# Kernel tuning notes

Hardware: AMD Instinct MI355X
Metric: run time of the kernel (lower is better)

The kernel has to match this reference:

```python
import jax, jax.numpy as jnp
import numpy as np

N = 50000   # nodes
E = 500000  # edges
H = 128     # hidden_dim


def setup_inputs() -> dict:
    key = jax.random.key(0)
    ks = jax.random.split(key, 8)
    w = lambda k, shp: jax.random.normal(k, shp, jnp.float32) * 0.02
    return {
        "edge_idx": jax.random.randint(ks[0], (E, 2), 0, N, dtype=jnp.int32),
        "node_feats": jax.random.normal(ks[1], (N, H), jnp.float32),
        "edge_feats": jax.random.normal(ks[2], (E, H), jnp.float32),
        # edge MLP params: Linear(3H,H) -> ReLU -> Linear(H,H) -> LayerNorm(H)
        "We1": w(ks[3], (3 * H, H)), "be1": jnp.zeros((H,), jnp.float32),
        "We2": w(ks[4], (H, H)),     "be2": jnp.zeros((H,), jnp.float32),
        "ge": jnp.ones((H,), jnp.float32), "bge": jnp.zeros((H,), jnp.float32),
        # node MLP params: Linear(2H,H) -> ReLU -> Linear(H,H) -> LayerNorm(H)
        "Wn1": w(ks[5], (2 * H, H)), "bn1": jnp.zeros((H,), jnp.float32),
        "Wn2": w(ks[6], (H, H)),     "bn2": jnp.zeros((H,), jnp.float32),
        "gn": jnp.ones((H,), jnp.float32), "bgn": jnp.zeros((H,), jnp.float32),
    }


def layer_norm(x, g, b, eps=1e-5):
    m = jnp.mean(x, axis=-1, keepdims=True)
    v = jnp.var(x, axis=-1, keepdims=True)
    return (x - m) * jax.lax.rsqrt(v + eps) * g + b


def reference(edge_idx, node_feats, edge_feats,
              We1, be1, We2, be2, ge, bge,
              Wn1, bn1, Wn2, bn2, gn, bgn):
    senders = edge_idx[:, 0]
    receivers = edge_idx[:, 1]
    # edge update: gather endpoints, concat with edge feats, MLP + LN
    e_in = jnp.concatenate([node_feats[senders], node_feats[receivers], edge_feats], axis=-1)  # [E, 3H]
    edge_update = layer_norm(jax.nn.relu(e_in @ We1 + be1) @ We2 + be2, ge, bge)               # [E, H]
    # faithful to source: scatter-add of edge_feats (NOT edge_update) into receivers
    acc = jax.ops.segment_sum(edge_feats, receivers, num_segments=node_feats.shape[0])          # [N, H]
    n_in = jnp.concatenate([node_feats, acc], axis=-1)                                          # [N, 2H]
    node_update = layer_norm(jax.nn.relu(n_in @ Wn1 + bn1) @ Wn2 + bn2, gn, bgn)                # [N, H]
    return node_feats + node_update, edge_feats + edge_update
```

## Files before the change

### kernel.cpp

```cpp
#include <hip/hip_runtime.h>
#include <hip/hip_bf16.h>

#define DI __device__ __forceinline__

typedef __attribute__((ext_vector_type(8))) short short8;
typedef __attribute__((ext_vector_type(4))) short short4v;
typedef __attribute__((ext_vector_type(4))) float floatx4;

constexpr int NN = 50000;
constexpr int NE = 500000;
constexpr int H  = 128;
constexpr int NB1 = (NN + 255) / 256;

constexpr size_t OFF_BF   = 229376;
constexpr size_t OFF_PS   = 294912;
constexpr size_t OFF_PR   = 13094912;
constexpr size_t OFF_CNT  = 25894912;
constexpr size_t OFF_TMP  = 26094912;
constexpr size_t OFF_RS   = 26294912;
constexpr size_t OFF_CUR  = 26494912;
constexpr size_t OFF_BSUM = 26694912;
constexpr size_t OFF_CSR  = 26695936;

constexpr int WF_TOTAL = 114688;
constexpr int BIASF_FLOATS = 8*2048;

DI short f2bf(float f){ __bf16 b = (__bf16)f; return __builtin_bit_cast(short, b); }
DI float bf2f(short s){ return __builtin_bit_cast(float, ((unsigned)(unsigned short)s) << 16); }

__global__ __launch_bounds__(256) void zero_cnt_kernel(int* __restrict__ cnt){
  int i = blockIdx.x*256 + threadIdx.x;
  if (i < NN) cnt[i] = 0;
}

__global__ __launch_bounds__(256) void prep_kernel(
    const float* __restrict__ We1, const float* __restrict__ We2,
    const float* __restrict__ Wn1, const float* __restrict__ Wn2,
    const float* __restrict__ be1, const float* __restrict__ be2,
    const float* __restrict__ ge,  const float* __restrict__ bge,
    const float* __restrict__ bn1, const float* __restrict__ bn2,
    const float* __restrict__ gn,  const float* __restrict__ bgn,
    short* __restrict__ wf, float* __restrict__ bf)
{
  int t = blockIdx.x*256 + threadIdx.x;
  if (t < WF_TOTAL) {
    int blk = t >> 14, u = t & 16383;
    int j = u & 7, l = (u>>3)&63, nt = (u>>9)&7, ks = u>>12;
    const float* src; int roff;
    switch (blk) {
      case 0: src = We1; roff = 0;   break;
      case 1: src = We1; roff = 128; break;
      case 2: src = We1; roff = 256; break;
      case 3: src = We2; roff = 0;   break;
      case 4: src = Wn1; roff = 0;   break;
      case 5: src = Wn1; roff = 128; break;
      default: src = Wn2; roff = 0;  break;
    }
    int row = roff + 32*ks + 8*(l>>4) + j;
    int col = 16*nt + (l&15);
    wf[t] = f2bf(src[row*H + col]);
  } else if (t < WF_TOTAL + BIASF_FLOATS) {
    int tb = t - WF_TOTAL;
    int arr = tb >> 11, u = tb & 2047;
    int r = u&3, l = (u>>2)&63, mt = u>>8;
    int feat = 16*mt + 4*(l>>4) + r;
    const float* s;
    switch (arr) {
      case 0: s = be1; break; case 1: s = be2; break;
      case 2: s = ge;  break; case 3: s = bge; break;
      case 4: s = bn1; break; case 5: s = bn2; break;
      case 6: s = gn;  break; default: s = bgn; break;
    }
    bf[tb] = s[feat];
  }
}

__global__ __launch_bounds__(256) void hist_kernel(const int* __restrict__ ei, int* __restrict__ cnt){
  int e = blockIdx.x*256 + threadIdx.x;
  if (e < NE) atomicAdd(&cnt[ei[2*e+1]], 1);
}

__global__ __launch_bounds__(256) void scan1_kernel(const int* __restrict__ cnt,
                                                    int* __restrict__ tmp, int* __restrict__ blocksum){
  __shared__ int s[256];
  int t = threadIdx.x, i = blockIdx.x*256 + t;
  int v = (i < NN) ? cnt[i] : 0;
  s[t] = v; __syncthreads();
#pragma unroll
  for (int o=1; o<256; o<<=1){
    int u = (t >= o) ? s[t-o] : 0;
    __syncthreads();
    s[t] += u;
    __syncthreads();
  }
  if (i < NN) tmp[i] = s[t];
  if (t == 255) blocksum[blockIdx.x] = s[255];
}

__global__ __launch_bounds__(256) void scan2_kernel(int* __restrict__ blocksum){
  __shared__ int s[256];
  int t = threadIdx.x;
  int v = (t < NB1) ? blocksum[t] : 0;
  s[t] = v; __syncthreads();
#pragma unroll
  for (int o=1; o<256; o<<=1){
    int u = (t >= o) ? s[t-o] : 0;
    __syncthreads();
    s[t] += u;
    __syncthreads();
  }
  if (t < NB1) blocksum[t] = s[t] - v;
}

__global__ __launch_bounds__(256) void scan3_kernel(const int* __restrict__ cnt, const int* __restrict__ tmp,
                                                    const int* __restrict__ blocksum,
                                                    int* __restrict__ rowstart, int* __restrict__ cursor){
  int i = blockIdx.x*256 + threadIdx.x;
  if (i < NN){
    int rs = tmp[i] - cnt[i] + blocksum[blockIdx.x];
    rowstart[i] = rs; cursor[i] = rs;
  }
}

__global__ __launch_bounds__(256) void scatter_kernel(const int* __restrict__ ei,
                                                      int* __restrict__ cursor, int* __restrict__ csr){
  int e = blockIdx.x*256 + threadIdx.x;
  if (e < NE){
    int r = ei[2*e+1];
    int p = atomicAdd(&cursor[r], 1);
    csr[p] = e;
  }
}

__global__ __launch_bounds__(256) void segsum_kernel(const int* __restrict__ csr,
                                                     const int* __restrict__ rowstart,
                                                     const int* __restrict__ cnt,
                                                     const float* __restrict__ edge_feats,
                                                     float* __restrict__ acc){
  int tid = threadIdx.x;
  int w = tid>>6, l = tid&63;
  int hh = l>>5, q = l&31;
  int n = blockIdx.x*8 + w*2 + hh;
  if (n >= NN) return;
  int start = rowstart[n], deg = cnt[n];
  floatx4 s = floatx4{0.f,0.f,0.f,0.f};
  int k = 0;
  for (; k+4 <= deg; k += 4){
    int e0 = csr[start+k],   e1 = csr[start+k+1];
    int e2 = csr[start+k+2], e3 = csr[start+k+3];
    floatx4 v0 = *(const floatx4*)(edge_feats + (size_t)e0*H + 4*q);
    floatx4 v1 = *(const floatx4*)(edge_feats + (size_t)e1*H + 4*q);
    floatx4 v2 = *(const floatx4*)(edge_feats + (size_t)e2*H + 4*q);
    floatx4 v3 = *(const floatx4*)(edge_feats + (size_t)e3*H + 4*q);
    s += v0; s += v1; s += v2; s += v3;
  }
  for (; k < deg; ++k){
    int e = csr[start+k];
    s += *(const floatx4*)(edge_feats + (size_t)e*H + 4*q);
  }
  *(floatx4*)(acc + (size_t)n*H + 4*q) = s;
}

__global__ __launch_bounds__(256) void pproj_kernel(
    const float* __restrict__ node_feats,
    const short* __restrict__ wsf, const short* __restrict__ wrf,
    const float* __restrict__ b1f,
    short* __restrict__ Ps, short* __restrict__ Pr)
{
  const int tid = threadIdx.x;
  const int w = tid>>6, l = tid&63, g = l>>4, lo = l&15;
  int row = blockIdx.x*64 + w*16 + lo;
  bool valid = row < NN;
  int rowc = valid ? row : (NN-1);
  const float* sp = node_feats + (size_t)rowc*H;

  short8 ein[4];
#pragma unroll
  for (int ks=0; ks<4; ++ks){
    const int koff = ks*32 + g*8;
    floatx4 f0 = *(const floatx4*)(sp + koff);
    floatx4 f1 = *(const floatx4*)(sp + koff + 4);
    ein[ks][0]=f2bf(f0[0]); ein[ks][1]=f2bf(f0[1]); ein[ks][2]=f2bf(f0[2]); ein[ks][3]=f2bf(f0[3]);
    ein[ks][4]=f2bf(f1[0]); ein[ks][5]=f2bf(f1[1]); ein[ks][6]=f2bf(f1[2]); ein[ks][7]=f2bf(f1[3]);
  }

  floatx4 as[8], ar[8];
#pragma unroll
  for (int mt=0; mt<8; ++mt){ as[mt] = floatx4{0,0,0,0}; ar[mt] = floatx4{0,0,0,0}; }
#pragma unroll
  for (int ks=0; ks<4; ++ks){
#pragma unroll
    for (int mt=0; mt<8; ++mt){
      short8 wv = *(const short8*)(wsf + ((ks*8+mt)*64 + l)*8);
      as[mt] = __builtin_amdgcn_mfma_f32_16x16x32_bf16(wv, ein[ks], as[mt], 0,0,0);
      short8 wv2 = *(const short8*)(wrf + ((ks*8+mt)*64 + l)*8);
      ar[mt] = __builtin_amdgcn_mfma_f32_16x16x32_bf16(wv2, ein[ks], ar[mt], 0,0,0);
    }
  }

  if (valid){
    short* ps = Ps + (size_t)rowc*H + g*32;
    short* pr = Pr + (size_t)rowc*H + g*32;
#pragma unroll
    for (int mt=0; mt<8; ++mt){
      floatx4 bv = *(const floatx4*)(b1f + (mt*64+l)*4);
      short4v vs, vr;
#pragma unroll
      for (int r=0; r<4; ++r){ vs[r] = f2bf(as[mt][r] + bv[r]); vr[r] = f2bf(ar[mt][r]); }
      *(short4v*)(ps + mt*4) = vs;
      *(short4v*)(pr + mt*4) = vr;
    }
  }
}

template<int R>
__global__ __launch_bounds__(256, 4) void edge_kernel(
    const int* __restrict__ edge_idx,
    const float* __restrict__ edge_feats,
    const short* __restrict__ Ps, const short* __restrict__ Pr,
    const short* __restrict__ wef, const short* __restrict__ w2f,
    const float* __restrict__ b2f,
    const float* __restrict__ gf,  const float* __restrict__ bgf,
    float* __restrict__ out_edge)
{
  __shared__ short lds_h[4*R*2048];
  const int tid = threadIdx.x;
  const int w = tid>>6, l = tid&63, g = l>>4, lo = l&15;

  int rowc[R]; bool valid[R]; int2 se[R];
#pragma unroll
  for (int b=0; b<R; ++b){
    int row = blockIdx.x*(64*R) + w*(16*R) + b*16 + lo;
    valid[b] = row < NE;
    rowc[b]  = valid[b] ? row : (NE-1);
    se[b] = *(const int2*)(edge_idx + 2*rowc[b]);
  }

  short8 vs[4], vr[4];
  {
    const short* ps = Ps + (size_t)se[0].x*H + g*32;
    const short* pr = Pr + (size_t)se[0].y*H + g*32;
#pragma unroll
    for (int m2=0; m2<4; ++m2){
      vs[m2] = *(const short8*)(ps + m2*8);
      vr[m2] = *(const short8*)(pr + m2*8);
    }
  }

#pragma unroll
  for (int b=0; b<R; ++b){
    floatx4 acc1[8];
#pragma unroll
    for (int mt=0; mt<8; ++mt) acc1[mt] = floatx4{0.f,0.f,0.f,0.f};

    const float* sp = edge_feats + (size_t)rowc[b]*H;
#pragma unroll
    for (int ks=0; ks<4; ++ks){
      const int koff = ks*32 + g*8;
      floatx4 f0 = *(const floatx4*)(sp + koff);
      floatx4 f1 = *(const floatx4*)(sp + koff + 4);
      short8 ein;
      ein[0]=f2bf(f0[0]); ein[1]=f2bf(f0[1]); ein[2]=f2bf(f0[2]); ein[3]=f2bf(f0[3]);
      ein[4]=f2bf(f1[0]); ein[5]=f2bf(f1[1]); ein[6]=f2bf(f1[2]); ein[7]=f2bf(f1[3]);
#pragma unroll
      for (int mt=0; mt<8; ++mt){
        short8 wv = *(const short8*)(wef + ((ks*8+mt)*64 + l)*8);
        acc1[mt] = __builtin_amdgcn_mfma_f32_16x16x32_bf16(wv, ein, acc1[mt], 0,0,0);
      }
    }

#pragma unroll
    for (int m2=0; m2<4; ++m2)
#pragma unroll
      for (int r=0; r<4; ++r){
        acc1[2*m2][r]   += bf2f(vs[m2][r])   + bf2f(vr[m2][r]);
        acc1[2*m2+1][r] += bf2f(vs[m2][4+r]) + bf2f(vr[m2][4+r]);
      }

    if (b+1 < R){
      const short* ps = Ps + (size_t)se[b+1].x*H + g*32;
      const short* pr = Pr + (size_t)se[b+1].y*H + g*32;
#pragma unroll
      for (int m2=0; m2<4; ++m2){
        vs[m2] = *(const short8*)(ps + m2*8);
        vr[m2] = *(const short8*)(pr + m2*8);
      }
    }

    short* ldsw = lds_h + (w*R + b)*2048;
#pragma unroll
    for (int mt=0; mt<8; ++mt){
      short4v hv;
#pragma unroll
      for (int r=0; r<4; ++r){
        float v = acc1[mt][r];
        hv[r] = f2bf(v > 0.f ? v : 0.f);
      }
      int off = (lo*256 + mt*32 + g*8) ^ ((lo&7)<<4);
      *(short4v*)((char*)ldsw + off) = hv;
    }
  }

  floatx4 acc2[R][8];
#pragma unroll
  for (int mt=0; mt<8; ++mt){
    floatx4 bv = *(const floatx4*)(b2f + (mt*64+l)*4);
#pragma unroll
    for (int b=0; b<R; ++b) acc2[b][mt] = bv;
  }

#pragma unroll
  for (int s=0; s<4; ++s){
    short8 hb[R];
#pragma unroll
    for (int b=0; b<R; ++b){
      short* ldsw = lds_h + (w*R + b)*2048;
      int roff = (lo*256 + s*64 + g*16) ^ ((lo&7)<<4);
      hb[b] = *(const short8*)((char*)ldsw + roff);
    }
#pragma unroll
    for (int mt=0; mt<8; ++mt){
      short8 wv = *(const short8*)(w2f + ((s*8+mt)*64 + l)*8);
#pragma unroll
      for (int b=0; b<R; ++b)
        acc2[b][mt] = __builtin_amdgcn_mfma_f32_16x16x32_bf16(wv, hb[b], acc2[b][mt], 0,0,0);
    }
  }

  float meanv[R], rsv[R];
#pragma unroll
  for (int b=0; b<R; ++b){
    float sum = 0.f, ssq = 0.f;
#pragma unroll
    for (int mt=0; mt<8; ++mt)
#pragma unroll
      for (int r=0; r<4; ++r){ float v = acc2[b][mt][r]; sum += v; ssq += v*v; }
    sum += __shfl_xor(sum, 16); ssq += __shfl_xor(ssq, 16);
    sum += __shfl_xor(sum, 32); ssq += __shfl_xor(ssq, 32);
    meanv[b] = sum * (1.f/H);
    float var = ssq * (1.f/H) - meanv[b]*meanv[b];
    rsv[b] = rsqrtf(var + 1e-5f);
  }

#pragma unroll
  for (int mt=0; mt<8; ++mt){
    floatx4 gv  = *(const floatx4*)(gf  + (mt*64+l)*4);
    floatx4 bgv = *(const floatx4*)(bgf + (mt*64+l)*4);
#pragma unroll
    for (int b=0; b<R; ++b){
      const float* resid = edge_feats + (size_t)rowc[b]*H;
      floatx4 ef = *(const floatx4*)(resid + mt*16 + g*4);
      floatx4 o;
#pragma unroll
      for (int r=0; r<4; ++r) o[r] = ef[r] + (acc2[b][mt][r]-meanv[b])*rsv[b]*gv[r] + bgv[r];
      if (valid[b]) *(floatx4*)(out_edge + (size_t)rowc[b]*H + mt*16 + g*4) = o;
    }
  }
}

__global__ __launch_bounds__(256) void node_kernel(
    const float* __restrict__ node_feats,
    const short* __restrict__ w1f, const short* __restrict__ w2f,
    const float* __restrict__ b1f, const float* __restrict__ b2f,
    const float* __restrict__ gf,  const float* __restrict__ bgf,
    float* __restrict__ out_node)
{
  __shared__ short lds_h[4*2048];
  const int tid = threadIdx.x;
  const int w = tid>>6, l = tid&63, g = l>>4, lo = l&15;
  short* ldsw = lds_h + w*2048;

  int row = blockIdx.x*64 + w*16 + lo;
  bool valid = row < NN;
  int rowc = valid ? row : (NN-1);
  const float* sp0 = node_feats + (size_t)rowc*H;
  const float* sp1 = out_node   + (size_t)rowc*H;

  floatx4 acc1[8];
#pragma unroll
  for (int mt=0; mt<8; ++mt) acc1[mt] = *(const floatx4*)(b1f + (mt*64+l)*4);

#pragma unroll
  for (int ks=0; ks<8; ++ks){
    const float* sp = (ks<4) ? sp0 : sp1;
    const int koff = (ks&3)*32 + g*8;
    floatx4 f0 = *(const floatx4*)(sp + koff);
    floatx4 f1 = *(const floatx4*)(sp + koff + 4);
    short8 ein;
    ein[0]=f2bf(f0[0]); ein[1]=f2bf(f0[1]); ein[2]=f2bf(f0[2]); ein[3]=f2bf(f0[3]);
    ein[4]=f2bf(f1[0]); ein[5]=f2bf(f1[1]); ein[6]=f2bf(f1[2]); ein[7]=f2bf(f1[3]);
#pragma unroll
    for (int mt=0; mt<8; ++mt){
      short8 wv = *(const short8*)(w1f + ((ks*8+mt)*64 + l)*8);
      acc1[mt] = __builtin_amdgcn_mfma_f32_16x16x32_bf16(wv, ein, acc1[mt], 0,0,0);
    }
  }

#pragma unroll
  for (int mt=0; mt<8; ++mt){
    short4v hv;
#pragma unroll
    for (int r=0; r<4; ++r){
      float v = acc1[mt][r];
      hv[r] = f2bf(v > 0.f ? v : 0.f);
    }
    int off = (lo*256 + mt*32 + g*8) ^ ((lo&7)<<4);
    *(short4v*)((char*)ldsw + off) = hv;
  }

  floatx4 acc2[8];
#pragma unroll
  for (int mt=0; mt<8; ++mt) acc2[mt] = *(const floatx4*)(b2f + (mt*64+l)*4);

#pragma unroll
  for (int s=0; s<4; ++s){
    int roff = (lo*256 + s*64 + g*16) ^ ((lo&7)<<4);
    short8 hb = *(const short8*)((char*)ldsw + roff);
#pragma unroll
    for (int mt=0; mt<8; ++mt){
      short8 wv = *(const short8*)(w2f + ((s*8+mt)*64 + l)*8);
      acc2[mt] = __builtin_amdgcn_mfma_f32_16x16x32_bf16(wv, hb, acc2[mt], 0,0,0);
    }
  }

  float sum = 0.f, ssq = 0.f;
#pragma unroll
  for (int mt=0; mt<8; ++mt)
#pragma unroll
    for (int r=0; r<4; ++r){ float v = acc2[mt][r]; sum += v; ssq += v*v; }
  sum += __shfl_xor(sum, 16); ssq += __shfl_xor(ssq, 16);
  sum += __shfl_xor(sum, 32); ssq += __shfl_xor(ssq, 32);
  const float mean = sum * (1.f/H);
  const float var  = ssq * (1.f/H) - mean*mean;
  const float rs   = rsqrtf(var + 1e-5f);

#pragma unroll
  for (int mt=0; mt<8; ++mt){
    floatx4 gv  = *(const floatx4*)(gf  + (mt*64+l)*4);
    floatx4 bgv = *(const floatx4*)(bgf + (mt*64+l)*4);
    floatx4 nf  = *(const floatx4*)(node_feats + (size_t)rowc*H + mt*16 + g*4);
    floatx4 o;
#pragma unroll
    for (int r=0; r<4; ++r) o[r] = nf[r] + (acc2[mt][r]-mean)*rs*gv[r] + bgv[r];
    if (valid) *(floatx4*)(out_node + (size_t)rowc*H + mt*16 + g*4) = o;
  }
}

extern "C" void kernel_launch(void* const* d_in, const int* in_sizes, int n_in,
                              void* d_out, int out_size, void* d_ws, size_t ws_size,
                              hipStream_t stream)
{
  const int*   edge_idx   = (const int*)  d_in[0];
  const float* node_feats = (const float*)d_in[1];
  const float* edge_feats = (const float*)d_in[2];
  const float* We1=(const float*)d_in[3];  const float* be1=(const float*)d_in[4];
  const float* We2=(const float*)d_in[5];  const float* be2=(const float*)d_in[6];
  const float* ge =(const float*)d_in[7];  const float* bge=(const float*)d_in[8];
  const float* Wn1=(const float*)d_in[9];  const float* bn1=(const float*)d_in[10];
  const float* Wn2=(const float*)d_in[11]; const float* bn2=(const float*)d_in[12];
  const float* gn =(const float*)d_in[13]; const float* bgn=(const float*)d_in[14];

  float* out_node = (float*)d_out;
  float* out_edge = out_node + (size_t)NN*H;

  char* ws = (char*)d_ws;
  short* wf      = (short*)ws;
  float* bf      = (float*)(ws + OFF_BF);
  short* Ps      = (short*)(ws + OFF_PS);
  short* Pr      = (short*)(ws + OFF_PR);
  int* cnt       = (int*)(ws + OFF_CNT);
  int* tmp       = (int*)(ws + OFF_TMP);
  int* rowstart  = (int*)(ws + OFF_RS);
  int* cursor    = (int*)(ws + OFF_CUR);
  int* blocksum  = (int*)(ws + OFF_BSUM);
  int* csr       = (int*)(ws + OFF_CSR);

  short* wsf  = wf;
  short* wrf  = wf + 16384;
  short* wef  = wf + 32768;
  short* w2f  = wf + 49152;
  short* wn1f = wf + 65536;
  short* wn2f = wf + 98304;
  float* b1f  = bf;         float* b2f  = bf + 2048;
  float* gef  = bf + 4096;  float* bgef = bf + 6144;
  float* bn1f = bf + 8192;  float* bn2f = bf + 10240;
  float* gnf  = bf + 12288; float* bgnf = bf + 14336;

  zero_cnt_kernel<<<NB1, 256, 0, stream>>>(cnt);
  prep_kernel<<<(WF_TOTAL + BIASF_FLOATS + 255)/256, 256, 0, stream>>>(
      We1, We2, Wn1, Wn2, be1, be2, ge, bge, bn1, bn2, gn, bgn, wf, bf);

  hist_kernel<<<(NE+255)/256, 256, 0, stream>>>(edge_idx, cnt);
  scan1_kernel<<<NB1, 256, 0, stream>>>(cnt, tmp, blocksum);
  scan2_kernel<<<1, 256, 0, stream>>>(blocksum);
  scan3_kernel<<<NB1, 256, 0, stream>>>(cnt, tmp, blocksum, rowstart, cursor);
  scatter_kernel<<<(NE+255)/256, 256, 0, stream>>>(edge_idx, cursor, csr);

  pproj_kernel<<<(NN+63)/64, 256, 0, stream>>>(node_feats, wsf, wrf, b1f, Ps, Pr);

  edge_kernel<2><<<(NE + 127)/128, 256, 0, stream>>>(
      edge_idx, edge_feats, Ps, Pr, wef, w2f, b2f, gef, bgef, out_edge);

  segsum_kernel<<<(NN+7)/8, 256, 0, stream>>>(csr, rowstart, cnt, edge_feats, out_node);

  node_kernel<<<(NN+63)/64, 256, 0, stream>>>(
      node_feats, wn1f, wn2f, bn1f, bn2f, gnf, bgnf, out_node);
}
```

Baseline: 438.9 us.

## Process edge sub-tiles fully sequentially to cut LDS and register footprint

The edge kernel now runs the second GEMM, LayerNorm and output write for each R sub-tile inside the per-sub-tile loop, instead of staging all R hidden tiles in LDS and keeping R sets of second-layer accumulators live. LDS shrinks to one 2048-short slab per wave and the acc2[R][8] register array goes away, which should lower VGPR and LDS pressure and allow more resident waves. The cost is that each W2 fragment is reloaded from global/cache once per sub-tile instead of being shared across R tiles, so there is less weight reuse per load.

Measured after the change: 793.7 us. 80.8% more time.

```diff
diff --git a/kernel.cpp b/kernel.cpp
--- a/kernel.cpp
+++ b/kernel.cpp
@@ -223,9 +223,10 @@
     const float* __restrict__ gf,  const float* __restrict__ bgf,
     float* __restrict__ out_edge)
 {
-  __shared__ short lds_h[4*R*2048];
+  __shared__ short lds_h[4*2048];
   const int tid = threadIdx.x;
   const int w = tid>>6, l = tid&63, g = l>>4, lo = l&15;
+  short* ldsw = lds_h + w*2048;
 
   int rowc[R]; bool valid[R]; int2 se[R];
 #pragma unroll
@@ -249,9 +250,9 @@
 
 #pragma unroll
   for (int b=0; b<R; ++b){
-    floatx4 acc1[8];
-#pragma unroll
-    for (int mt=0; mt<8; ++mt) acc1[mt] = floatx4{0.f,0.f,0.f,0.f};
+    floatx4 acc[8];
+#pragma unroll
+    for (int mt=0; mt<8; ++mt) acc[mt] = floatx4{0.f,0.f,0.f,0.f};
 
     const float* sp = edge_feats + (size_t)rowc[b]*H;
 #pragma unroll
@@ -265,7 +266,7 @@
 #pragma unroll
       for (int mt=0; mt<8; ++mt){
         short8 wv = *(const short8*)(wef + ((ks*8+mt)*64 + l)*8);
-        acc1[mt] = __builtin_amdgcn_mfma_f32_16x16x32_bf16(wv, ein, acc1[mt], 0,0,0);
+        acc[mt] = __builtin_amdgcn_mfma_f32_16x16x32_bf16(wv, ein, acc[mt], 0,0,0);
       }
     }
 
@@ -273,8 +274,8 @@
     for (int m2=0; m2<4; ++m2)
 #pragma unroll
       for (int r=0; r<4; ++r){
-        acc1[2*m2][r]   += bf2f(vs[m2][r])   + bf2f(vr[m2][r]);
-        acc1[2*m2+1][r] += bf2f(vs[m2][4+r]) + bf2f(vr[m2][4+r]);
+        acc[2*m2][r]   += bf2f(vs[m2][r])   + bf2f(vr[m2][r]);
+        acc[2*m2+1][r] += bf2f(vs[m2][4+r]) + bf2f(vr[m2][4+r]);
       }
 
     if (b+1 < R){
@@ -287,73 +288,54 @@
       }
     }
 
-    short* ldsw = lds_h + (w*R + b)*2048;
 #pragma unroll
     for (int mt=0; mt<8; ++mt){
       short4v hv;
 #pragma unroll
       for (int r=0; r<4; ++r){
-        float v = acc1[mt][r];
+        float v = acc[mt][r];
         hv[r] = f2bf(v > 0.f ? v : 0.f);
       }
       int off = (lo*256 + mt*32 + g*8) ^ ((lo&7)<<4);
       *(short4v*)((char*)ldsw + off) = hv;
     }
-  }
-
-  floatx4 acc2[R][8];
-#pragma unroll
-  for (int mt=0; mt<8; ++mt){
-    floatx4 bv = *(const floatx4*)(b2f + (mt*64+l)*4);
-#pragma unroll
-    for (int b=0; b<R; ++b) acc2[b][mt] = bv;
-  }
-
-#pragma unroll
-  for (int s=0; s<4; ++s){
-    short8 hb[R];
-#pragma unroll
-    for (int b=0; b<R; ++b){
-      short* ldsw = lds_h + (w*R + b)*2048;
+
+#pragma unroll
+    for (int mt=0; mt<8; ++mt) acc[mt] = *(const floatx4*)(b2f + (mt*64+l)*4);
+
+#pragma unroll
+    for (int s=0; s<4; ++s){
       int roff = (lo*256 + s*64 + g*16) ^ ((lo&7)<<4);
-      hb[b] = *(const short8*)((char*)ldsw + roff);
-    }
-#pragma unroll
-    for (int mt=0; mt<8; ++mt){
-      short8 wv = *(const short8*)(w2f + ((s*8+mt)*64 + l)*8);
-#pragma unroll
-      for (int b=0; b<R; ++b)
-        acc2[b][mt] = __builtin_amdgcn_mfma_f32_16x16x32_bf16(wv, hb[b], acc2[b][mt], 0,0,0);
-    }
-  }
-
-  float meanv[R], rsv[R];
-#pragma unroll
-  for (int b=0; b<R; ++b){
+      short8 hb = *(const short8*)((char*)ldsw + roff);
+#pragma unroll
+      for (int mt=0; mt<8; ++mt){
+        short8 wv = *(const short8*)(w2f + ((s*8+mt)*64 + l)*8);
+        acc[mt] = __builtin_amdgcn_mfma_f32_16x16x32_bf16(wv, hb, acc[mt], 0,0,0);
+      }
+    }
+
     float sum = 0.f, ssq = 0.f;
 #pragma unroll
     for (int mt=0; mt<8; ++mt)
 #pragma unroll
-      for (int r=0; r<4; ++r){ float v = acc2[b][mt][r]; sum += v; ssq += v*v; }
+      for (int r=0; r<4; ++r){ float v = acc[mt][r]; sum += v; ssq += v*v; }
     sum += __shfl_xor(sum, 16); ssq += __shfl_xor(ssq, 16);
     sum += __shfl_xor(sum, 32); ssq += __shfl_xor(ssq, 32);
-    meanv[b] = sum * (1.f/H);
-    float var = ssq * (1.f/H) - meanv[b]*meanv[b];
-    rsv[b] = rsqrtf(var + 1e-5f);
-  }
-
-#pragma unroll
-  for (int mt=0; mt<8; ++mt){
-    floatx4 gv  = *(const floatx4*)(gf  + (mt*64+l)*4);
-    floatx4 bgv = *(const floatx4*)(bgf + (mt*64+l)*4);
-#pragma unroll
-    for (int b=0; b<R; ++b){
-      const float* resid = edge_feats + (size_t)rowc[b]*H;
-      floatx4 ef = *(const floatx4*)(resid + mt*16 + g*4);
+    const float mean = sum * (1.f/H);
+    const float var  = ssq * (1.f/H) - mean*mean;
+    const float rs   = rsqrtf(var + 1e-5f);
+
+    const float* resid = edge_feats + (size_t)rowc[b]*H;
+    float* outp = out_edge + (size_t)rowc[b]*H;
+#pragma unroll
+    for (int mt=0; mt<8; ++mt){
+      floatx4 gv  = *(const floatx4*)(gf  + (mt*64+l)*4);
+      floatx4 bgv = *(const floatx4*)(bgf + (mt*64+l)*4);
+      floatx4 ef  = *(const floatx4*)(resid + mt*16 + g*4);
       floatx4 o;
 #pragma unroll
-      for (int r=0; r<4; ++r) o[r] = ef[r] + (acc2[b][mt][r]-meanv[b])*rsv[b]*gv[r] + bgv[r];
-      if (valid[b]) *(floatx4*)(out_edge + (size_t)rowc[b]*H + mt*16 + g*4) = o;
+      for (int r=0; r<4; ++r) o[r] = ef[r] + (acc[mt][r]-mean)*rs*gv[r] + bgv[r];
+      if (valid[b]) *(floatx4*)(outp + mt*16 + g*4) = o;
     }
   }
 }
```
